# Optimization experiments

Measured on AMD Instinct MI355X. Metric: run time of the kernel, lower is better.

The kernel has to match this reference:

```python
import jax, jax.numpy as jnp
import numpy as np

VTH = 0.5      # SNNParameters.vth_init
TAU = 0.25     # SNNParameters.tau_mem
_GAUSS_C = 1.0 / np.sqrt(0.3 * np.pi)  # surrogate-grad scale (unused in fwd)


def _heaviside(v):
    return (v > 0).astype(v.dtype)


def setup_inputs() -> dict:
    key = jax.random.key(0)
    x = jax.random.normal(key, (16, 128, 512, 32), dtype=jnp.float32)
    return {"x": x}


def reference(x):
    # x: [..., T]; LIF recurrence over the last (time) axis.
    xT = jnp.moveaxis(x, -1, 0)  # [T, ...]
    u0 = jnp.zeros(x.shape[:-1], dtype=x.dtype)
    o0 = jnp.zeros(x.shape[:-1], dtype=x.dtype)

    def step(carry, x_t):
        u, o_prev = carry
        u = TAU * u * (1.0 - o_prev) + x_t          # leaky integrate w/ reset
        o = _heaviside(u - VTH)                     # fire
        return (u, o), o

    _, outT = jax.lax.scan(step, (u0, o0), xT)
    return jnp.moveaxis(outT, 0, -1)  # back to [..., T]
```

## Files before the change

### kernel.cpp

```cpp
#include <hip/hip_runtime.h>


constexpr int T = 32;
constexpr float TAU = 0.25f;
constexpr float VTH = 0.5f;
constexpr int QUADS_PER_ROW = T / 4;
constexpr int TILE_F4 = 256 * QUADS_PER_ROW;

__device__ __forceinline__ int swz(int s) { return s ^ ((s >> 3) & 7); }

__global__ __launch_bounds__(256) void LIFSpike_kernel(
    const float* __restrict__ x, float* __restrict__ out) {
    __shared__ float4 tile[TILE_F4];

    const int t = threadIdx.x;
    const size_t base = (size_t)blockIdx.x * TILE_F4;

    const float4* __restrict__ xp = reinterpret_cast<const float4*>(x);
#pragma unroll
    for (int k = 0; k < QUADS_PER_ROW; ++k) {
        int s = k * 256 + t;
        tile[swz(s)] = xp[base + s];
    }
    __syncthreads();

    float u = 0.0f, o = 0.0f;
#pragma unroll
    for (int j = 0; j < QUADS_PER_ROW; ++j) {
        int phys = t * QUADS_PER_ROW + (j ^ (t & 7));
        float4 v = tile[phys];
        float4 r;

        u = TAU * u * (1.0f - o) + v.x;
        o = (u > VTH) ? 1.0f : 0.0f;
        r.x = o;

        u = TAU * u * (1.0f - o) + v.y;
        o = (u > VTH) ? 1.0f : 0.0f;
        r.y = o;

        u = TAU * u * (1.0f - o) + v.z;
        o = (u > VTH) ? 1.0f : 0.0f;
        r.z = o;

        u = TAU * u * (1.0f - o) + v.w;
        o = (u > VTH) ? 1.0f : 0.0f;
        r.w = o;

        tile[phys] = r;
    }
    __syncthreads();

    float4* __restrict__ op = reinterpret_cast<float4*>(out);
#pragma unroll
    for (int k = 0; k < QUADS_PER_ROW; ++k) {
        int s = k * 256 + t;
        op[base + s] = tile[swz(s)];
    }
}

extern "C" void kernel_launch(void* const* d_in, const int* in_sizes, int n_in,
                              void* d_out, int out_size, void* d_ws, size_t ws_size,
                              hipStream_t stream) {
    const float* x = (const float*)d_in[0];
    float* out = (float*)d_out;
    int total_f4 = in_sizes[0] / 4;
    int grid = total_f4 / TILE_F4;
    LIFSpike_kernel<<<grid, 256, 0, stream>>>(x, out);
}
```

Measured before the change: 229.7 us.

## Drop LDS staging; load rows directly into registers with software prefetch

```diff
diff --git a/kernel.cpp b/kernel.cpp
--- a/kernel.cpp
+++ b/kernel.cpp
@@ -1,70 +1,68 @@
 #include <hip/hip_runtime.h>
 
+
+typedef float fx4 __attribute__((ext_vector_type(4)));
 
 constexpr int T = 32;
 constexpr float TAU = 0.25f;
 constexpr float VTH = 0.5f;
-constexpr int QUADS_PER_ROW = T / 4;
-constexpr int TILE_F4 = 256 * QUADS_PER_ROW;
+constexpr int QPR = T / 4;
+constexpr int RPT = 4;
+constexpr int BLOCK = 256;
+constexpr int ROWS_PER_BLOCK = BLOCK * RPT;
 
-__device__ __forceinline__ int swz(int s) { return s ^ ((s >> 3) & 7); }
+__global__ __launch_bounds__(BLOCK) void LIFSpike_kernel(
+    const fx4* __restrict__ x, fx4* __restrict__ out) {
+    const int nb = gridDim.x;
+    const int b = blockIdx.x;
+    const int chunk = (b & 7) * (nb >> 3) + (b >> 3);
+    const size_t row0 = (size_t)chunk * ROWS_PER_BLOCK + threadIdx.x;
 
-__global__ __launch_bounds__(256) void LIFSpike_kernel(
-    const float* __restrict__ x, float* __restrict__ out) {
-    __shared__ float4 tile[TILE_F4];
+    fx4 cur[QPR], nxt[QPR];
+    const fx4* p0 = x + row0 * QPR;
+#pragma unroll
+    for (int j = 0; j < QPR; ++j) cur[j] = p0[j];
 
-    const int t = threadIdx.x;
-    const size_t base = (size_t)blockIdx.x * TILE_F4;
+#pragma unroll
+    for (int k = 0; k < RPT; ++k) {
+        if (k + 1 < RPT) {
+            const fx4* pn = x + (row0 + (size_t)(k + 1) * BLOCK) * QPR;
+#pragma unroll
+            for (int j = 0; j < QPR; ++j) nxt[j] = pn[j];
+        }
 
-    const float4* __restrict__ xp = reinterpret_cast<const float4*>(x);
+        fx4* po = out + (row0 + (size_t)k * BLOCK) * QPR;
+        float u = 0.0f, o = 0.0f;
 #pragma unroll
-    for (int k = 0; k < QUADS_PER_ROW; ++k) {
-        int s = k * 256 + t;
-        tile[swz(s)] = xp[base + s];
-    }
-    __syncthreads();
+        for (int j = 0; j < QPR; ++j) {
+            fx4 v = cur[j];
+            fx4 r;
+            u = TAU * u * (1.0f - o) + v.x;
+            o = (u > VTH) ? 1.0f : 0.0f;
+            r.x = o;
+            u = TAU * u * (1.0f - o) + v.y;
+            o = (u > VTH) ? 1.0f : 0.0f;
+            r.y = o;
+            u = TAU * u * (1.0f - o) + v.z;
+            o = (u > VTH) ? 1.0f : 0.0f;
+            r.z = o;
+            u = TAU * u * (1.0f - o) + v.w;
+            o = (u > VTH) ? 1.0f : 0.0f;
+            r.w = o;
+            __builtin_nontemporal_store(r, po + j);
+        }
 
-    float u = 0.0f, o = 0.0f;
 #pragma unroll
-    for (int j = 0; j < QUADS_PER_ROW; ++j) {
-        int phys = t * QUADS_PER_ROW + (j ^ (t & 7));
-        float4 v = tile[phys];
-        float4 r;
-
-        u = TAU * u * (1.0f - o) + v.x;
-        o = (u > VTH) ? 1.0f : 0.0f;
-        r.x = o;
-
-        u = TAU * u * (1.0f - o) + v.y;
-        o = (u > VTH) ? 1.0f : 0.0f;
-        r.y = o;
-
-        u = TAU * u * (1.0f - o) + v.z;
-        o = (u > VTH) ? 1.0f : 0.0f;
-        r.z = o;
-
-        u = TAU * u * (1.0f - o) + v.w;
-        o = (u > VTH) ? 1.0f : 0.0f;
-        r.w = o;
-
-        tile[phys] = r;
-    }
-    __syncthreads();
-
-    float4* __restrict__ op = reinterpret_cast<float4*>(out);
-#pragma unroll
-    for (int k = 0; k < QUADS_PER_ROW; ++k) {
-        int s = k * 256 + t;
-        op[base + s] = tile[swz(s)];
+        for (int j = 0; j < QPR; ++j) cur[j] = nxt[j];
     }
 }
 
 extern "C" void kernel_launch(void* const* d_in, const int* in_sizes, int n_in,
                               void* d_out, int out_size, void* d_ws, size_t ws_size,
                               hipStream_t stream) {
-    const float* x = (const float*)d_in[0];
-    float* out = (float*)d_out;
-    int total_f4 = in_sizes[0] / 4;
-    int grid = total_f4 / TILE_F4;
-    LIFSpike_kernel<<<grid, 256, 0, stream>>>(x, out);
+    const fx4* x = (const fx4*)d_in[0];
+    fx4* out = (fx4*)d_out;
+    int n_rows = in_sizes[0] / T;
+    int grid = n_rows / ROWS_PER_BLOCK;
+    LIFSpike_kernel<<<grid, BLOCK, 0, stream>>>(x, out);
 }
```

Result: slower. 532.8 us (+131.9%).
